# Optimization experiments

Hardware: AMD Instinct MI355X
Metric: run time of the kernel (lower is better)

Reference implementation:

```python
import math
import jax, jax.numpy as jnp
import numpy as np

EPS = 1e-5
SCALE_BASE = 512.0


def xpos_apply(x, downscale=False):
    # x: (..., L, head_dim); faithful to RetNet's XPOS (torchscale xpos)
    L, hd = x.shape[-2], x.shape[-1]
    half = hd // 2
    scale_vec = (jnp.arange(0, hd, 2, dtype=x.dtype) + 0.4 * hd) / (1.4 * hd)  # (half,)
    pos = jnp.arange(L, dtype=x.dtype)
    scale = scale_vec[None, :] ** (pos[:, None] / SCALE_BASE)  # (L, half)
    inv_freq = 1.0 / (10000.0 ** (jnp.arange(half, dtype=x.dtype) / half))
    sinusoid = pos[:, None] * inv_freq[None, :]  # (L, half)
    sin, cos = jnp.sin(sinusoid), jnp.cos(sinusoid)
    if downscale:
        scale = 1.0 / scale
    dup = lambda m: jnp.repeat(m, 2, axis=-1)  # duplicate_interleave -> (L, hd)
    sin_s, cos_s = dup(sin * scale), dup(cos * scale)
    x1, x2 = x[..., ::2], x[..., 1::2]
    rot = jnp.stack((-x2, x1), axis=-1).reshape(x.shape)  # rotate_every_two
    return x * cos_s + rot * sin_s


def decay_mask(L, gammas, dtype):
    # D[h, n, m] = gamma_h ** (n - m) if n >= m else 0
    n = jnp.arange(L)[:, None]
    m = jnp.arange(L)[None, :]
    causal = n >= m
    dist = jnp.where(causal, (n - m).astype(dtype), 0.0)
    return jnp.where(causal, gammas[:, None, None] ** dist, 0.0)  # (H, L, L)


def setup_inputs() -> dict:
    key = jax.random.key(0)
    ks = jax.random.split(key, 7)
    B, L, D, H = 1, 4096, 512, 8
    hs = D // H  # head_size = head_v_dim (double_v_dim=False)
    v_dim = D
    X = jax.random.normal(ks[0], (B, L, D), jnp.float32)
    W_Q = jax.random.normal(ks[1], (H, D, hs), jnp.float32) / D
    W_K = jax.random.normal(ks[2], (H, D, hs), jnp.float32) / D
    W_V = jax.random.normal(ks[3], (H, D, hs), jnp.float32) / D
    W_G = jax.random.normal(ks[4], (D, v_dim), jnp.float32) / D
    W_O = jax.random.normal(ks[5], (v_dim, D), jnp.float32) / D
    gn_weight = jnp.ones((v_dim,), jnp.float32)
    gn_bias = jnp.zeros((v_dim,), jnp.float32)
    return {"X": X, "W_Q": W_Q, "W_K": W_K, "W_V": W_V,
            "W_G": W_G, "W_O": W_O, "gn_weight": gn_weight, "gn_bias": gn_bias}


def reference(X, W_Q, W_K, W_V, W_G, W_O, gn_weight, gn_bias):
    B, L, D = X.shape
    H, _, hs = W_Q.shape
    hv = W_V.shape[-1]
    # per-head projections
    q = jnp.einsum('bld,ndh->bnlh', X, W_Q)
    k = jnp.einsum('bld,ndh->bnlh', X, W_K)
    v = jnp.einsum('bld,ndv->bnlv', X, W_V)
    q = xpos_apply(q, downscale=False)
    k = xpos_apply(k, downscale=True)
    # fixed (non-trainable) decay gammas: 1 - exp(linspace(log(1/32), log(1/512)))
    gammas = 1.0 - jnp.exp(jnp.linspace(math.log(1.0 / 32), math.log(1.0 / 512), H)).astype(X.dtype)
    Dmask = decay_mask(L, gammas, X.dtype)  # (H, L, L)
    scores = jnp.einsum('bnlh,bnsh->bnls', q, k) * Dmask[None]
    ret = jnp.einsum('bnls,bnsv->bnlv', scores, v)
    ret = ret.transpose(0, 2, 1, 3).reshape(B, L, H * hv)  # b l (n h)
    # GroupNorm(heads, v_dim) applied to (B*L, v_dim)
    g = ret.reshape(B * L, H, hv)
    mu = g.mean(-1, keepdims=True)
    var = g.var(-1, keepdims=True)
    g = (g - mu) * jax.lax.rsqrt(var + EPS)
    g = g.reshape(B, L, H * hv) * gn_weight + gn_bias
    gate = jax.nn.silu(X @ W_G)
    return (gate * g) @ W_O
```

## Files before the change

### kernel.cpp

```cpp
#include <hip/hip_runtime.h>
#include <math.h>

#define LQ 4096
#define DD 512
#define NH 8
#define HS 64
#define HALF 32

typedef unsigned short u16;
typedef unsigned int u32;
typedef __attribute__((ext_vector_type(8)))  short s8v;
typedef __attribute__((ext_vector_type(4)))  float f4v;
typedef __attribute__((ext_vector_type(4)))  u32  u32x4;
typedef __attribute__((ext_vector_type(16))) float f16v;

#define WS_QH   0u
#define WS_QL   1048576u
#define WS_KH   2097152u
#define WS_KL   3145728u
#define WS_VT   4194304u
#define WS_XFH  5242880u
#define WS_XFL  6291456u
#define WS_WF   7340032u
#define WS_GATE 8650752u
#define WS_TAB  10747904u
#define WS_KTWH 11272192u
#define WS_KTWL 12320768u

__device__ inline u16 f2bf(float x) {
    unsigned int u = __float_as_uint(x);
    return (u16)((u + 0x7fffu + ((u >> 16) & 1u)) >> 16);
}
__device__ inline float bf2f(u16 h) { return __uint_as_float(((unsigned int)h) << 16); }

__device__ __forceinline__ void gld16(void* lds, const void* g) {
    __builtin_amdgcn_global_load_lds(
        (const __attribute__((address_space(1))) void*)g,
        (__attribute__((address_space(3))) void*)lds, 16, 0, 0);
}

__global__ __launch_bounds__(256) void k_pre(
    const float* __restrict__ X,
    const float* __restrict__ Wq, const float* __restrict__ Wk, const float* __restrict__ Wv,
    const float* __restrict__ Wg, const float* __restrict__ Wo,
    float* __restrict__ tab, u16* __restrict__ Xfh, u16* __restrict__ Xfl,
    u16* __restrict__ Wf) {
    __shared__ float tile[32][33];
    const int b = blockIdx.x;
    const int t = threadIdx.x;
    if (b < 512) {
        int idx = b * 256 + t;
        if (idx >= LQ * HALF) return;
        int l = idx >> 5;
        int i = idx & 31;
        double log2sv = log2((2.0 * i + 25.6) / 89.6);
        double e = (double)l * log2sv * (1.0 / 512.0);
        float sc  = exp2f((float)e);
        float sci = exp2f((float)(-e));
        double invf = exp2((double)i * (-13.287712379549449 / 32.0));
        double th = (double)l * invf;
        double r = th - 6.283185307179586 * floor(th * 0.15915494309189535);
        float c = cosf((float)r), sn = sinf((float)r);
        tab[idx]                 = c * sc;
        tab[LQ*HALF + idx]       = sn * sc;
        tab[2*LQ*HALF + idx]     = c * sci;
        tab[3*LQ*HALF + idx]     = sn * sci;
    } else if (b < 1536) {
        int g = (b - 512) * 256 + t;
        int l = g >> 6;
        int d = (g & 63) * 8;
        const float* xp = X + (size_t)l * DD + d;
        f4v x0 = *(const f4v*)xp;
        f4v x1 = *(const f4v*)(xp + 4);
        s8v ph, pl;
#pragma unroll
        for (int j = 0; j < 4; ++j) {
            u16 hb = f2bf(x0[j]);
            ph[j] = (short)hb; pl[j] = (short)f2bf(x0[j] - bf2f(hb));
            u16 hb2 = f2bf(x1[j]);
            ph[j+4] = (short)hb2; pl[j+4] = (short)f2bf(x1[j] - bf2f(hb2));
        }
        int rb = l >> 5, kt = d >> 6, ks = (d >> 4) & 3, kh2 = (d >> 3) & 1;
        int lane = kh2 * 32 + (l & 31);
        size_t off = (((size_t)(rb * 8 + kt) * 4 + ks) * 64 + lane) * 8;
        *(s8v*)(Xfh + off) = ph;
        *(s8v*)(Xfl + off) = pl;
    } else {
        int bb = b - 1536;
        int d0 = (bb & 15) * 32, C0 = (bb >> 4) * 32;
        int proj = C0 >> 9;
        int tc = t & 31, tr = t >> 5;
#pragma unroll
        for (int rr = 0; rr < 4; ++rr) {
            int dl = tr + rr * 8;
            int d = d0 + dl;
            int C = C0 + tc;
            float val;
            if (proj < 3) {
                const float* W = (proj == 0) ? Wq : ((proj == 1) ? Wk : Wv);
                int h = (C & 511) >> 6, hs = C & 63;
                val = W[(size_t)h * (DD * HS) + (size_t)d * HS + hs];
            } else if (proj == 3) {
                val = Wg[(size_t)d * DD + (C & 511)];
            } else {
                val = Wo[(size_t)d * DD + (C - 2048)];
            }
            tile[dl][tc] = val;
        }
        __syncthreads();
        if (t < 128) {
            int cl = t & 31, dgq = t >> 5;
            int dl = dgq * 8;
            s8v pk;
#pragma unroll
            for (int j = 0; j < 8; ++j) pk[j] = (short)f2bf(tile[dl + j][cl]);
            int C = C0 + cl;
            int da = d0 + dl;
            int nb = C >> 5, kt = da >> 6, ks = (da >> 4) & 3, kh2 = (da >> 3) & 1;
            int lane = kh2 * 32 + (C & 31);
            size_t off = (((size_t)(nb * 8 + kt) * 4 + ks) * 64 + lane) * 8;
            *(s8v*)(Wf + off) = pk;
        }
    }
}

__global__ __launch_bounds__(256) void k_fused(
    const u16* __restrict__ Xfh, const u16* __restrict__ Xfl,
    const u16* __restrict__ Wf,
    const float* __restrict__ tab,
    u16* __restrict__ qh, u16* __restrict__ ql,
    u16* __restrict__ kh, u16* __restrict__ kl,
    u16* __restrict__ vt, u16* __restrict__ gate16,
    u16* __restrict__ ktwh, u16* __restrict__ ktwl) {
    __shared__ __align__(16) char smem[33024];
    const int t = threadIdx.x;
    const int b = blockIdx.x;
    const int mb = (b & 7) * 4 + (b >> 8);
    const int cb = (b >> 3) & 31;
    const int l0 = mb * 128;
    const int c0 = cb * 64;
    const int wv = t >> 6;
    const int lane = t & 63;
    const int c31 = lane & 31;
    const int hi = lane >> 5;

    const int rb = mb * 4 + wv;
    const u16* pAh = Xfh + (size_t)rb * 16384 + lane * 8;
    const u16* pAl = Xfl + (size_t)rb * 16384 + lane * 8;
    const char* gB = (const char*)(Wf + (size_t)(cb * 2) * 16384);

    f16v acc0, acc1;
#pragma unroll
    for (int i = 0; i < 16; ++i) { acc0[i] = 0.f; acc1[i] = 0.f; }

#define STAGEB(PH)                                                             \
    { _Pragma("unroll") for (int j = 0; j < 8; ++j) {                          \
        int seg = j >> 2, q4 = j & 3;                                          \
        gld16(smem + seg * 16384 + q4 * 4096 + wv * 1024,                      \
              gB + seg * 32768 + (PH) * 16384 + q4 * 4096 + t * 16); } }

    if (c0 < 1024) {
        s8v ahA[4], alA[4], ahB[4], alB[4];
#define LOADQ(S, KT)                                                      \
        { _Pragma("unroll") for (int ks = 0; ks < 4; ++ks) {              \
            ah##S[ks] = *(const s8v*)(pAh + (KT) * 2048 + ks * 512);      \
            al##S[ks] = *(const s8v*)(pAl + (KT) * 2048 + ks * 512); } }
#define MFMAQ(S, KT)                                                                        \
        { const char* bbq = smem + ((KT) & 3) * 4096;                                       \
          _Pragma("unroll") for (int ks = 0; ks < 4; ++ks) {                                \
            s8v b0 = *(const s8v*)(bbq + ks * 1024 + lane * 16);                            \
            s8v b1 = *(const s8v*)(bbq + 16384 + ks * 1024 + lane * 16);                    \
            acc0 = __builtin_amdgcn_mfma_f32_32x32x16_bf16(ah##S[ks], b0, acc0, 0, 0, 0);   \
            acc0 = __builtin_amdgcn_mfma_f32_32x32x16_bf16(al##S[ks], b0, acc0, 0, 0, 0);   \
            acc1 = __builtin_amdgcn_mfma_f32_32x32x16_bf16(ah##S[ks], b1, acc1, 0, 0, 0);   \
            acc1 = __builtin_amdgcn_mfma_f32_32x32x16_bf16(al##S[ks], b1, acc1, 0, 0, 0); } }
        STAGEB(0)
        LOADQ(A, 0)
        asm volatile("s_waitcnt vmcnt(0)" ::: "memory");
        __syncthreads();
        LOADQ(B, 1)
        __builtin_amdgcn_sched_barrier(0);
        MFMAQ(A, 0)
        LOADQ(A, 2)
        __builtin_amdgcn_sched_barrier(0);
        MFMAQ(B, 1)
        LOADQ(B, 3)
        __builtin_amdgcn_sched_barrier(0);
        MFMAQ(A, 2)
        LOADQ(A, 4)
        __builtin_amdgcn_sched_barrier(0);
        MFMAQ(B, 3)
        __syncthreads();
        STAGEB(1)
        asm volatile("s_waitcnt vmcnt(0)" ::: "memory");
        __syncthreads();
        LOADQ(B, 5)
        __builtin_amdgcn_sched_barrier(0);
        MFMAQ(A, 4)
        LOADQ(A, 6)
        __builtin_amdgcn_sched_barrier(0);
        MFMAQ(B, 5)
        LOADQ(B, 7)
        __builtin_amdgcn_sched_barrier(0);
        MFMAQ(A, 6)
        __builtin_amdgcn_sched_barrier(0);
        MFMAQ(B, 7)
#undef LOADQ
#undef MFMAQ
    } else {
        s8v ahA[4], ahB[4];
#define LOADS(S, KT)                                                      \
        { _Pragma("unroll") for (int ks = 0; ks < 4; ++ks) {              \
            ah##S[ks] = *(const s8v*)(pAh + (KT) * 2048 + ks * 512); } }
#define MFMAS(S, KT)                                                                        \
        { const char* bbq = smem + ((KT) & 3) * 4096;                                       \
          _Pragma("unroll") for (int ks = 0; ks < 4; ++ks) {                                \
            s8v b0 = *(const s8v*)(bbq + ks * 1024 + lane * 16);                            \
            s8v b1 = *(const s8v*)(bbq + 16384 + ks * 1024 + lane * 16);                    \
            acc0 = __builtin_amdgcn_mfma_f32_32x32x16_bf16(ah##S[ks], b0, acc0, 0, 0, 0);   \
            acc1 = __builtin_amdgcn_mfma_f32_32x32x16_bf16(ah##S[ks], b1, acc1, 0, 0, 0); } }
        STAGEB(0)
        LOADS(A, 0)
        asm volatile("s_waitcnt vmcnt(0)" ::: "memory");
        __syncthreads();
        LOADS(B, 1)
        __builtin_amdgcn_sched_barrier(0);
        MFMAS(A, 0)
        LOADS(A, 2)
        __builtin_amdgcn_sched_barrier(0);
        MFMAS(B, 1)
        LOADS(B, 3)
        __builtin_amdgcn_sched_barrier(0);
        MFMAS(A, 2)
        LOADS(A, 4)
        __builtin_amdgcn_sched_barrier(0);
        MFMAS(B, 3)
        __syncthreads();
        STAGEB(1)
        asm volatile("s_waitcnt vmcnt(0)" ::: "memory");
        __syncthreads();
        LOADS(B, 5)
        __builtin_amdgcn_sched_barrier(0);
        MFMAS(A, 4)
        LOADS(A, 6)
        __builtin_amdgcn_sched_barrier(0);
        MFMAS(B, 5)
        LOADS(B, 7)
        __builtin_amdgcn_sched_barrier(0);
        MFMAS(A, 6)
        __builtin_amdgcn_sched_barrier(0);
        MFMAS(B, 7)
#undef LOADS
#undef MFMAS
    }
#undef STAGEB
    __syncthreads();

    float* vbuf = (float*)smem;
    const int proj = c0 >> 9;
    if (proj < 2) {
        const float* ct = tab + (proj ? 2 * LQ * HALF : 0);
        const float* st = tab + (proj ? 3 * LQ * HALF : LQ * HALF);
        u16* oh = proj ? kh : qh;
        u16* ol = proj ? kl : ql;
        const int hh = (c0 & 511) >> 6;
        float lgf = 0.f;
        if (proj == 1) {
            double lg = -3.4657359027997265 + (double)hh * (-2.772588722239781 / 7.0);
            lgf = (float)(log(1.0 - exp(lg)) * 1.4426950408889634);
        }
#pragma unroll
        for (int n = 0; n < 2; ++n) {
            const f16v acc = n ? acc1 : acc0;
            int C = c0 + n * 32 + c31;
            int hs = C & 63, i2 = hs >> 1;
            float sgn = (hs & 1) ? 1.f : -1.f;
#pragma unroll
            for (int r = 0; r < 16; ++r) {
                int lrow = wv * 32 + (r & 3) + 8 * (r >> 2) + 4 * hi;
                int pos = l0 + lrow;
                float val = acc[r];
                float part = __shfl_xor(val, 1);
                float res = val * ct[pos * HALF + i2] + sgn * part * st[pos * HALF + i2];
                u16 hb = f2bf(res);
                size_t o = ((size_t)hh * LQ + pos) * HS + hs;
                oh[o] = hb;
                ol[o] = f2bf(res - bf2f(hb));
                if (proj == 1) {
                    float wf = exp2f(lgf * (float)(64 - (pos & 63)));
                    vbuf[(n * 32 + c31) * 129 + lrow] = res * wf;
                }
            }
        }
        if (proj == 1) {
            __syncthreads();
            int cl = t >> 2, lseg = (t & 3) * 32;
            size_t o = ((size_t)hh * HS + cl) * LQ + l0 + lseg;
#pragma unroll
            for (int ch4 = 0; ch4 < 4; ++ch4) {
                s8v pkh, pkl;
#pragma unroll
                for (int j = 0; j < 8; ++j) {
                    float v = vbuf[cl * 129 + lseg + ch4 * 8 + j];
                    u16 hb = f2bf(v);
                    pkh[j] = (short)hb;
                    pkl[j] = (short)f2bf(v - bf2f(hb));
                }
                *(s8v*)(ktwh + o + ch4 * 8) = pkh;
                *(s8v*)(ktwl + o + ch4 * 8) = pkl;
            }
        }
    } else if (proj == 2) {
#pragma unroll
        for (int n = 0; n < 2; ++n) {
            const f16v acc = n ? acc1 : acc0;
            int cl = n * 32 + c31;
#pragma unroll
            for (int r = 0; r < 16; ++r) {
                int lrow = wv * 32 + (r & 3) + 8 * (r >> 2) + 4 * hi;
                vbuf[cl * 129 + lrow] = acc[r];
            }
        }
        __syncthreads();
        int h = (c0 & 511) >> 6;
        int cl = t >> 2, lseg = (t & 3) * 32;
        size_t o = ((size_t)h * HS + cl) * LQ + l0 + lseg;
#pragma unroll
        for (int ch = 0; ch < 4; ++ch) {
            s8v pk;
#pragma unroll
            for (int j = 0; j < 8; ++j) pk[j] = (short)f2bf(vbuf[cl * 129 + lseg + ch * 8 + j]);
            *(s8v*)(vt + o + ch * 8) = pk;
        }
    } else {
#pragma unroll
        for (int n = 0; n < 2; ++n) {
            const f16v acc = n ? acc1 : acc0;
            int C = (c0 & 511) + n * 32 + c31;
#pragma unroll
            for (int r = 0; r < 16; ++r) {
                int lrow = wv * 32 + (r & 3) + 8 * (r >> 2) + 4 * hi;
                float vv = acc[r];
                gate16[(size_t)(l0 + lrow) * DD + C] = f2bf(vv / (1.f + expf(-vv)));
            }
        }
    }
}

__global__ __launch_bounds__(256) void k_ret1(
    const u16* __restrict__ vt, const u16* __restrict__ ktwh, const u16* __restrict__ ktwl,
    float* __restrict__ A) {
    const int t = threadIdx.x;
    const int c = blockIdx.x;
    const int h = blockIdx.y;
    const int wv = t >> 6, lane = t & 63, c31 = lane & 31, hi = lane >> 5;
    const int wch = wv >> 1, wd = wv & 1;

    s8v va[4];
    const u16* vp = vt + ((size_t)h * 64 + wch * 32 + c31) * LQ + c * 64 + hi * 8;
#pragma unroll
    for (int ks = 0; ks < 4; ++ks) va[ks] = *(const s8v*)(vp + ks * 16);

    f16v a;
#pragma unroll
    for (int i = 0; i < 16; ++i) a[i] = 0.f;

    const size_t kbase = ((size_t)h * 64 + wd * 32 + c31) * LQ + c * 64 + hi * 8;
#pragma unroll
    for (int ks = 0; ks < 4; ++ks) {
        s8v b_h = *(const s8v*)(ktwh + kbase + ks * 16);
        s8v b_l = *(const s8v*)(ktwl + kbase + ks * 16);
        a = __builtin_amdgcn_mfma_f32_32x32x16_bf16(va[ks], b_h, a, 0, 0, 0);
        a = __builtin_amdgcn_mfma_f32_32x32x16_bf16(va[ks], b_l, a, 0, 0, 0);
    }

    float* Ab = A + ((size_t)h * 64 + c) * 4096;
#pragma unroll
    for (int r = 0; r < 16; ++r) {
        int ch = wch * 32 + (r & 3) + 8 * (r >> 2) + 4 * hi;
        Ab[ch * 64 + wd * 32 + c31] = a[r];
    }
}

__global__ __launch_bounds__(256) void k_scan(
    const float* __restrict__ A, u16* __restrict__ sth, u16* __restrict__ stl) {
    const int bx = blockIdx.x;
    const int h = bx >> 4;
    const int e = (bx & 15) * 256 + threadIdx.x;
    double lg = -3.4657359027997265 + (double)h * (-2.772588722239781 / 7.0);
    double gamma = 1.0 - exp(lg);
    float g64 = (float)pow(gamma, 64.0);
    const float* Ab = A + (size_t)h * 64 * 4096 + e;
    u16* shb = sth + (size_t)h * 64 * 4096 + e;
    u16* slb = stl + (size_t)h * 64 * 4096 + e;
    float av[64];
#pragma unroll
    for (int cc = 0; cc < 64; ++cc) av[cc] = Ab[(size_t)cc * 4096];
    float s = 0.f;
#pragma unroll
    for (int cc = 0; cc < 64; ++cc) {
        if (cc) {
            u16 hb = f2bf(s);
            shb[(size_t)cc * 4096] = hb;
            slb[(size_t)cc * 4096] = f2bf(s - bf2f(hb));
        }
        s = fmaf(g64, s, av[cc]);
    }
}

__global__ __launch_bounds__(256) void k_ret3(
    const u16* __restrict__ qh, const u16* __restrict__ ql,
    const u16* __restrict__ kh, const u16* __restrict__ kl,
    const u16* __restrict__ vt,
    const u16* __restrict__ sth, const u16* __restrict__ stl,
    const u16* __restrict__ gate16,
    const float* __restrict__ gw, const float* __restrict__ gb,
    u16* __restrict__ Gf) {
    __shared__ __align__(16) char sBuf[24576];
    __shared__ float stats[64][2][2];
    const int t = threadIdx.x;
    const int c = blockIdx.x;
    const int h = blockIdx.y;
    const int wv = t >> 6, lane = t & 63, c31 = lane & 31, hi = lane >> 5;
    const int ws = wv >> 1, wc = wv & 1;
    const int l0q = c * 64;

    double lg = -3.4657359027997265 + (double)h * (-2.772588722239781 / 7.0);
    double gamma = 1.0 - exp(lg);
    float lgf = (float)(log(gamma) * 1.4426950408889634);
    float c1a[4], c8a[4];
#pragma unroll
    for (int m = 0; m < 4; ++m) { c1a[m] = exp2f(-lgf * (float)m); c8a[m] = exp2f(-lgf * (float)(8 * m)); }

    s8v qhf[4], qlf[4];
    {
        const u16* qph = qh + ((size_t)h * LQ + l0q + ws * 32 + c31) * HS + hi * 8;
        const u16* qpl = ql + ((size_t)h * LQ + l0q + ws * 32 + c31) * HS + hi * 8;
#pragma unroll
        for (int ks = 0; ks < 4; ++ks) {
            qhf[ks] = *(const s8v*)(qph + ks * 16);
            qlf[ks] = *(const s8v*)(qpl + ks * 16);
        }
    }

    {
        const char* gKH = (const char*)kh + ((size_t)h * LQ + l0q) * 128;
        const char* gKL = (const char*)kl + ((size_t)h * LQ + l0q) * 128;
        const char* gVT = (const char*)vt + ((size_t)h * 64) * 8192 + l0q * 2;
#pragma unroll
        for (int i_ = 0; i_ < 6; ++i_) {
            int boff = i_ * 4096 + t * 16;
            int seg = boff >> 13;
            int o_ = boff & 8191;
            int osrc = o_ ^ (((o_ >> 7) & 7) << 4);
            const char* src = (seg == 0) ? gKH + osrc
                            : (seg == 1) ? gKL + osrc
                            : gVT + (size_t)(osrc >> 7) * 8192 + (osrc & 127);
            gld16(sBuf + (i_ & ~0) * 4096 + (t >> 6) * 1024, src);
        }
    }

    f16v qs;
#pragma unroll
    for (int i = 0; i < 16; ++i) qs[i] = 0.f;
    if (c > 0) {
        const u16* sbh = sth + ((size_t)h * 64 + c) * 4096;
        const u16* sbl = stl + ((size_t)h * 64 + c) * 4096;
#pragma unroll
        for (int ks = 0; ks < 4; ++ks) {
            int off = (wc * 32 + c31) * 64 + ks * 16 + hi * 8;
            s8v b_h = *(const s8v*)(sbh + off);
            s8v b_l = *(const s8v*)(sbl + off);
            qs = __builtin_amdgcn_mfma_f32_32x32x16_bf16(qhf[ks], b_h, qs, 0, 0, 0);
            qs = __builtin_amdgcn_mfma_f32_32x32x16_bf16(qhf[ks], b_l, qs, 0, 0, 0);
            qs = __builtin_amdgcn_mfma_f32_32x32x16_bf16(qlf[ks], b_h, qs, 0, 0, 0);
        }
    }

    asm volatile("s_waitcnt vmcnt(0)" ::: "memory");
    __syncthreads();

    f16v acc;
#pragma unroll
    for (int i = 0; i < 16; ++i) acc[i] = 0.f;
    const char* bKH = sBuf;
    const char* bKL = sBuf + 8192;
    const char* bVT = sBuf + 16384;

#pragma unroll
    for (int jt = 0; jt < 2; ++jt) {
        if (ws == 0 && jt == 1) break;
        f16v sacc;
#pragma unroll
        for (int i = 0; i < 16; ++i) sacc[i] = 0.f;
#pragma unroll
        for (int ks = 0; ks < 4; ++ks) {
            int krow = jt * 32 + c31;
            int ph = krow * 128 + ((ks * 32 + hi * 16) ^ ((krow & 7) << 4));
            s8v ah = *(const s8v*)(bKH + ph);
            s8v al = *(const s8v*)(bKL + ph);
            sacc = __builtin_amdgcn_mfma_f32_32x32x16_bf16(ah, qhf[ks], sacc, 0, 0, 0);
            sacc = __builtin_amdgcn_mfma_f32_32x32x16_bf16(ah, qlf[ks], sacc, 0, 0, 0);
            sacc = __builtin_amdgcn_mfma_f32_32x32x16_bf16(al, qhf[ks], sacc, 0, 0, 0);
        }
        const int D0 = (ws * 32 + c31) - jt * 32;
        float base = exp2f(lgf * (float)(D0 - 4 * hi));
        u32 w[8];
#pragma unroll
        for (int g = 0; g < 4; ++g) {
            float wg = base * c8a[g];
            float v0 = sacc[4 * g + 0] * (wg * c1a[0]);
            float v1 = sacc[4 * g + 1] * (wg * c1a[1]);
            float v2 = sacc[4 * g + 2] * (wg * c1a[2]);
            float v3 = sacc[4 * g + 3] * (wg * c1a[3]);
            int jr = 8 * g + 4 * hi;
            if (D0 - (jr + 0) < 0) v0 = 0.f;
            if (D0 - (jr + 1) < 0) v1 = 0.f;
            if (D0 - (jr + 2) < 0) v2 = 0.f;
            if (D0 - (jr + 3) < 0) v3 = 0.f;
            w[2 * g]     = (u32)f2bf(v0) | ((u32)f2bf(v1) << 16);
            w[2 * g + 1] = (u32)f2bf(v2) | ((u32)f2bf(v3) << 16);
        }
        u32 e0 = __shfl_xor(hi ? w[0] : w[2], 32);
        u32 e1 = __shfl_xor(hi ? w[1] : w[3], 32);
        u32 e2 = __shfl_xor(hi ? w[4] : w[6], 32);
        u32 e3 = __shfl_xor(hi ? w[5] : w[7], 32);
        u32x4 a0v = { hi ? e0 : w[0], hi ? e1 : w[1], hi ? w[2] : e0, hi ? w[3] : e1 };
        u32x4 a1v = { hi ? e2 : w[4], hi ? e3 : w[5], hi ? w[6] : e2, hi ? w[7] : e3 };
        s8v af0 = __builtin_bit_cast(s8v, a0v);
        s8v af1 = __builtin_bit_cast(s8v, a1v);
#pragma unroll
        for (int ksl = 0; ksl < 2; ++ksl) {
            s8v af = ksl ? af1 : af0;
            int cb = (jt * 2 + ksl) * 32 + hi * 16;
            int rv = wc * 32 + c31;
            s8v vb = *(const s8v*)(bVT + rv * 128 + (cb ^ ((rv & 7) << 4)));
            acc = __builtin_amdgcn_mfma_f32_32x32x16_bf16(af, vb, acc, 0, 0, 0);
        }
    }

    float vv[16];
#pragma unroll
    for (int r = 0; r < 16; ++r) {
        int row = (r & 3) + 8 * (r >> 2) + 4 * hi;
        int nloc = ws * 32 + row;
        float sc = exp2f(lgf * (float)nloc);
        vv[r] = acc[r] + sc * qs[r];
    }
#pragma unroll
    for (int r = 0; r < 16; ++r) {
        float s = vv[r], ss = vv[r] * vv[r];
#pragma unroll
        for (int off = 1; off < 32; off <<= 1) {
            s  += __shfl_xor(s, off);
            ss += __shfl_xor(ss, off);
        }
        if (c31 == 0) {
            int nloc = ws * 32 + (r & 3) + 8 * (r >> 2) + 4 * hi;
            stats[nloc][wc][0] = s;
            stats[nloc][wc][1] = ss;
        }
    }
    __syncthreads();

    float* gT = (float*)sBuf;
    const float gwv = gw[h * HS + wc * 32 + c31];
    const float gbv = gb[h * HS + wc * 32 + c31];
#pragma unroll
    for (int r = 0; r < 16; ++r) {
        int nloc = ws * 32 + (r & 3) + 8 * (r >> 2) + 4 * hi;
        float s  = stats[nloc][0][0] + stats[nloc][1][0];
        float ss = stats[nloc][0][1] + stats[nloc][1][1];
        float mean = s * (1.f / 64.f);
        float var = ss * (1.f / 64.f) - mean * mean;
        float inv = rsqrtf(var + 1e-5f);
        size_t o = (size_t)(l0q + nloc) * DD + h * HS + wc * 32 + c31;
        float g = ((vv[r] - mean) * inv * gwv + gbv) * bf2f(gate16[o]);
        gT[nloc * 65 + wc * 32 + c31] = g;
    }
    __syncthreads();
#pragma unroll
    for (int i = 0; i < 2; ++i) {
        int u = t + i * 256;
        int rbl = u >> 8;
        int ks = (u >> 6) & 3;
        int ln = u & 63;
        int row = rbl * 32 + (ln & 31);
        int ch = ks * 16 + (ln >> 5) * 8;
        s8v pk;
#pragma unroll
        for (int j = 0; j < 8; ++j) pk[j] = (short)f2bf(gT[row * 65 + ch + j]);
        size_t off = ((((size_t)(c * 2 + rbl) * 8 + h) * 4 + ks) * 64 + ln) * 8;
        *(s8v*)(Gf + off) = pk;
    }
}

__global__ __launch_bounds__(256) void k_out(
    const u16* __restrict__ Gf, const u16* __restrict__ Wf,
    float* __restrict__ out) {
    __shared__ __align__(16) char smem[32768];
    const int t = threadIdx.x;
    const int l0 = blockIdx.x * 128;
    const int c0 = blockIdx.y * 64;
    const int wv = t >> 6;
    const int lane = t & 63;
    const int c31 = lane & 31;
    const int hi = lane >> 5;

    const int rb = blockIdx.x * 4 + wv;
    const u16* pA  = Gf + (size_t)rb * 16384 + lane * 8;
    const char* gB = (const char*)(Wf + (size_t)(64 + blockIdx.y * 2) * 16384);

    f16v acc0, acc1;
#pragma unroll
    for (int i = 0; i < 16; ++i) { acc0[i] = 0.f; acc1[i] = 0.f; }

#define STAGEB(PH)                                                             \
    { _Pragma("unroll") for (int j = 0; j < 8; ++j) {                          \
        int seg = j >> 2, q4 = j & 3;                                          \
        gld16(smem + seg * 16384 + q4 * 4096 + wv * 1024,                      \
              gB + seg * 32768 + (PH) * 16384 + q4 * 4096 + t * 16); } }
    s8v aA[4], aB[4];
#define LOADO(S, KT)                                                      \
    { _Pragma("unroll") for (int ks = 0; ks < 4; ++ks) {                  \
        a##S[ks] = *(const s8v*)(pA + (KT) * 2048 + ks * 512); } }
#define MFMAO(S, KT)                                                                        \
    { const char* bbq = smem + ((KT) & 3) * 4096;                                           \
      _Pragma("unroll") for (int ks = 0; ks < 4; ++ks) {                                    \
        s8v b0 = *(const s8v*)(bbq + ks * 1024 + lane * 16);                                \
        s8v b1 = *(const s8v*)(bbq + 16384 + ks * 1024 + lane * 16);                        \
        acc0 = __builtin_amdgcn_mfma_f32_32x32x16_bf16(a##S[ks], b0, acc0, 0, 0, 0);        \
        acc1 = __builtin_amdgcn_mfma_f32_32x32x16_bf16(a##S[ks], b1, acc1, 0, 0, 0); } }
    STAGEB(0)
    LOADO(A, 0)
    asm volatile("s_waitcnt vmcnt(0)" ::: "memory");
    __syncthreads();
    LOADO(B, 1)
    __builtin_amdgcn_sched_barrier(0);
    MFMAO(A, 0)
    LOADO(A, 2)
    __builtin_amdgcn_sched_barrier(0);
    MFMAO(B, 1)
    LOADO(B, 3)
    __builtin_amdgcn_sched_barrier(0);
    MFMAO(A, 2)
    LOADO(A, 4)
    __builtin_amdgcn_sched_barrier(0);
    MFMAO(B, 3)
    __syncthreads();
    STAGEB(1)
    asm volatile("s_waitcnt vmcnt(0)" ::: "memory");
    __syncthreads();
    LOADO(B, 5)
    __builtin_amdgcn_sched_barrier(0);
    MFMAO(A, 4)
    LOADO(A, 6)
    __builtin_amdgcn_sched_barrier(0);
    MFMAO(B, 5)
    LOADO(B, 7)
    __builtin_amdgcn_sched_barrier(0);
    MFMAO(A, 6)
    __builtin_amdgcn_sched_barrier(0);
    MFMAO(B, 7)
#undef LOADO
#undef MFMAO
#undef STAGEB

#pragma unroll
    for (int n = 0; n < 2; ++n) {
        const f16v acc = n ? acc1 : acc0;
        int C = c0 + n * 32 + c31;
#pragma unroll
        for (int r = 0; r < 16; ++r) {
            int lrow = wv * 32 + (r & 3) + 8 * (r >> 2) + 4 * hi;
            out[(size_t)(l0 + lrow) * DD + C] = acc[r];
        }
    }
}

extern "C" void kernel_launch(void* const* d_in, const int* in_sizes, int n_in,
                              void* d_out, int out_size, void* d_ws, size_t ws_size,
                              hipStream_t stream) {
    const float* X   = (const float*)d_in[0];
    const float* W_Q = (const float*)d_in[1];
    const float* W_K = (const float*)d_in[2];
    const float* W_V = (const float*)d_in[3];
    const float* W_G = (const float*)d_in[4];
    const float* W_O = (const float*)d_in[5];
    const float* gnw = (const float*)d_in[6];
    const float* gnb = (const float*)d_in[7];

    float* ws   = (float*)d_ws;
    u16* qhp  = (u16*)(ws + WS_QH);
    u16* qlp  = (u16*)(ws + WS_QL);
    u16* khp  = (u16*)(ws + WS_KH);
    u16* klp  = (u16*)(ws + WS_KL);
    u16* vtp  = (u16*)(ws + WS_VT);
    u16* xfh  = (u16*)(ws + WS_XFH);
    u16* xfl  = (u16*)(ws + WS_XFL);
    u16* wf   = (u16*)(ws + WS_WF);
    u16* gate16 = (u16*)(ws + WS_GATE);
    float* tab  = ws + WS_TAB;
    u16* ktwh = (u16*)(ws + WS_KTWH);
    u16* ktwl = (u16*)(ws + WS_KTWL);
    float* Abuf = ws + WS_XFH;
    u16* sthp = (u16*)(ws + WS_KTWH);
    u16* stlp = (u16*)(ws + WS_KTWL);
    u16* Gfp  = (u16*)(ws + WS_XFH);
    float* out  = (float*)d_out;

    k_pre<<<2816, 256, 0, stream>>>(X, W_Q, W_K, W_V, W_G, W_O, tab, xfh, xfl, wf);
    k_fused<<<1024, 256, 0, stream>>>(xfh, xfl, wf, tab, qhp, qlp, khp, klp, vtp, gate16, ktwh, ktwl);
    k_ret1<<<dim3(64, 8), 256, 0, stream>>>(vtp, ktwh, ktwl, Abuf);
    k_scan<<<128, 256, 0, stream>>>(Abuf, sthp, stlp);
    k_ret3<<<dim3(64, 8), 256, 0, stream>>>(qhp, qlp, khp, klp, vtp, sthp, stlp,
                                            gate16, gnw, gnb, Gfp);
    k_out<<<dim3(32, 8), 256, 0, stream>>>(Gfp, wf, out);
}
```

Before: 78.54 us.

## Drop split-bf16 hi/lo compensation and use single bf16 operands throughout

Removes the hi/lo bf16 error-compensation split from every stage: X, Q, K, the decayed K tile, and the scan states are now stored as a single bf16. The extra MFMAs on the low-part terms are dropped, along with the low-part buffers, their loads and their LDS staging. This cuts MFMA work, memory traffic and shared memory use across the projection, retention, scan and chunk kernels. The cost is lower numerical accuracy, which risks failing the tolerance check against the fp32 reference.

```diff
diff --git a/kernel.cpp b/kernel.cpp
--- a/kernel.cpp
+++ b/kernel.cpp
@@ -15,7 +15,6 @@
 typedef __attribute__((ext_vector_type(16))) float f16v;
 
 #define WS_QH   0u
-#define WS_QL   1048576u
 #define WS_KH   2097152u
 #define WS_KL   3145728u
 #define WS_VT   4194304u
@@ -25,7 +24,6 @@
 #define WS_GATE 8650752u
 #define WS_TAB  10747904u
 #define WS_KTWH 11272192u
-#define WS_KTWL 12320768u
 
 __device__ inline u16 f2bf(float x) {
     unsigned int u = __float_as_uint(x);
@@ -43,8 +41,7 @@
     const float* __restrict__ X,
     const float* __restrict__ Wq, const float* __restrict__ Wk, const float* __restrict__ Wv,
     const float* __restrict__ Wg, const float* __restrict__ Wo,
-    float* __restrict__ tab, u16* __restrict__ Xfh, u16* __restrict__ Xfl,
-    u16* __restrict__ Wf) {
+    float* __restrict__ tab, u16* __restrict__ Xf, u16* __restrict__ Wf) {
     __shared__ float tile[32][33];
     const int b = blockIdx.x;
     const int t = threadIdx.x;
@@ -72,19 +69,16 @@
         const float* xp = X + (size_t)l * DD + d;
         f4v x0 = *(const f4v*)xp;
         f4v x1 = *(const f4v*)(xp + 4);
-        s8v ph, pl;
+        s8v ph;
 #pragma unroll
         for (int j = 0; j < 4; ++j) {
-            u16 hb = f2bf(x0[j]);
-            ph[j] = (short)hb; pl[j] = (short)f2bf(x0[j] - bf2f(hb));
-            u16 hb2 = f2bf(x1[j]);
-            ph[j+4] = (short)hb2; pl[j+4] = (short)f2bf(x1[j] - bf2f(hb2));
+            ph[j]   = (short)f2bf(x0[j]);
+            ph[j+4] = (short)f2bf(x1[j]);
         }
         int rb = l >> 5, kt = d >> 6, ks = (d >> 4) & 3, kh2 = (d >> 3) & 1;
         int lane = kh2 * 32 + (l & 31);
         size_t off = (((size_t)(rb * 8 + kt) * 4 + ks) * 64 + lane) * 8;
-        *(s8v*)(Xfh + off) = ph;
-        *(s8v*)(Xfl + off) = pl;
+        *(s8v*)(Xf + off) = ph;
     } else {
         int bb = b - 1536;
         int d0 = (bb & 15) * 32, C0 = (bb >> 4) * 32;
@@ -125,13 +119,11 @@
 }
 
 __global__ __launch_bounds__(256) void k_fused(
-    const u16* __restrict__ Xfh, const u16* __restrict__ Xfl,
-    const u16* __restrict__ Wf,
+    const u16* __restrict__ Xf, const u16* __restrict__ Wf,
     const float* __restrict__ tab,
-    u16* __restrict__ qh, u16* __restrict__ ql,
-    u16* __restrict__ kh, u16* __restrict__ kl,
+    u16* __restrict__ qh, u16* __restrict__ kh,
     u16* __restrict__ vt, u16* __restrict__ gate16,
-    u16* __restrict__ ktwh, u16* __restrict__ ktwl) {
+    u16* __restrict__ ktw) {
     __shared__ __align__(16) char smem[33024];
     const int t = threadIdx.x;
     const int b = blockIdx.x;
@@ -145,8 +137,7 @@
     const int hi = lane >> 5;
 
     const int rb = mb * 4 + wv;
-    const u16* pAh = Xfh + (size_t)rb * 16384 + lane * 8;
-    const u16* pAl = Xfl + (size_t)rb * 16384 + lane * 8;
+    const u16* pA = Xf + (size_t)rb * 16384 + lane * 8;
     const char* gB = (const char*)(Wf + (size_t)(cb * 2) * 16384);
 
     f16v acc0, acc1;
@@ -158,101 +149,50 @@
         int seg = j >> 2, q4 = j & 3;                                          \
         gld16(smem + seg * 16384 + q4 * 4096 + wv * 1024,                      \
               gB + seg * 32768 + (PH) * 16384 + q4 * 4096 + t * 16); } }
-
-    if (c0 < 1024) {
-        s8v ahA[4], alA[4], ahB[4], alB[4];
-#define LOADQ(S, KT)                                                      \
-        { _Pragma("unroll") for (int ks = 0; ks < 4; ++ks) {              \
-            ah##S[ks] = *(const s8v*)(pAh + (KT) * 2048 + ks * 512);      \
-            al##S[ks] = *(const s8v*)(pAl + (KT) * 2048 + ks * 512); } }
-#define MFMAQ(S, KT)                                                                        \
-        { const char* bbq = smem + ((KT) & 3) * 4096;                                       \
-          _Pragma("unroll") for (int ks = 0; ks < 4; ++ks) {                                \
-            s8v b0 = *(const s8v*)(bbq + ks * 1024 + lane * 16);                            \
-            s8v b1 = *(const s8v*)(bbq + 16384 + ks * 1024 + lane * 16);                    \
-            acc0 = __builtin_amdgcn_mfma_f32_32x32x16_bf16(ah##S[ks], b0, acc0, 0, 0, 0);   \
-            acc0 = __builtin_amdgcn_mfma_f32_32x32x16_bf16(al##S[ks], b0, acc0, 0, 0, 0);   \
-            acc1 = __builtin_amdgcn_mfma_f32_32x32x16_bf16(ah##S[ks], b1, acc1, 0, 0, 0);   \
-            acc1 = __builtin_amdgcn_mfma_f32_32x32x16_bf16(al##S[ks], b1, acc1, 0, 0, 0); } }
-        STAGEB(0)
-        LOADQ(A, 0)
-        asm volatile("s_waitcnt vmcnt(0)" ::: "memory");
-        __syncthreads();
-        LOADQ(B, 1)
-        __builtin_amdgcn_sched_barrier(0);
-        MFMAQ(A, 0)
-        LOADQ(A, 2)
-        __builtin_amdgcn_sched_barrier(0);
-        MFMAQ(B, 1)
-        LOADQ(B, 3)
-        __builtin_amdgcn_sched_barrier(0);
-        MFMAQ(A, 2)
-        LOADQ(A, 4)
-        __builtin_amdgcn_sched_barrier(0);
-        MFMAQ(B, 3)
-        __syncthreads();
-        STAGEB(1)
-        asm volatile("s_waitcnt vmcnt(0)" ::: "memory");
-        __syncthreads();
-        LOADQ(B, 5)
-        __builtin_amdgcn_sched_barrier(0);
-        MFMAQ(A, 4)
-        LOADQ(A, 6)
-        __builtin_amdgcn_sched_barrier(0);
-        MFMAQ(B, 5)
-        LOADQ(B, 7)
-        __builtin_amdgcn_sched_barrier(0);
-        MFMAQ(A, 6)
-        __builtin_amdgcn_sched_barrier(0);
-        MFMAQ(B, 7)
-#undef LOADQ
-#undef MFMAQ
-    } else {
-        s8v ahA[4], ahB[4];
-#define LOADS(S, KT)                                                      \
-        { _Pragma("unroll") for (int ks = 0; ks < 4; ++ks) {              \
-            ah##S[ks] = *(const s8v*)(pAh + (KT) * 2048 + ks * 512); } }
-#define MFMAS(S, KT)                                                                        \
-        { const char* bbq = smem + ((KT) & 3) * 4096;                                       \
-          _Pragma("unroll") for (int ks = 0; ks < 4; ++ks) {                                \
-            s8v b0 = *(const s8v*)(bbq + ks * 1024 + lane * 16);                            \
-            s8v b1 = *(const s8v*)(bbq + 16384 + ks * 1024 + lane * 16);                    \
-            acc0 = __builtin_amdgcn_mfma_f32_32x32x16_bf16(ah##S[ks], b0, acc0, 0, 0, 0);   \
-            acc1 = __builtin_amdgcn_mfma_f32_32x32x16_bf16(ah##S[ks], b1, acc1, 0, 0, 0); } }
-        STAGEB(0)
-        LOADS(A, 0)
-        asm volatile("s_waitcnt vmcnt(0)" ::: "memory");
-        __syncthreads();
-        LOADS(B, 1)
-        __builtin_amdgcn_sched_barrier(0);
-        MFMAS(A, 0)
-        LOADS(A, 2)
-        __builtin_amdgcn_sched_barrier(0);
-        MFMAS(B, 1)
-        LOADS(B, 3)
-        __builtin_amdgcn_sched_barrier(0);
-        MFMAS(A, 2)
-        LOADS(A, 4)
-        __builtin_amdgcn_sched_barrier(0);
-        MFMAS(B, 3)
-        __syncthreads();
-        STAGEB(1)
-        asm volatile("s_waitcnt vmcnt(0)" ::: "memory");
-        __syncthreads();
-        LOADS(B, 5)
-        __builtin_amdgcn_sched_barrier(0);
-        MFMAS(A, 4)
-        LOADS(A, 6)
-        __builtin_amdgcn_sched_barrier(0);
-        MFMAS(B, 5)
-        LOADS(B, 7)
-        __builtin_amdgcn_sched_barrier(0);
-        MFMAS(A, 6)
-        __builtin_amdgcn_sched_barrier(0);
-        MFMAS(B, 7)
-#undef LOADS
-#undef MFMAS
-    }
+    s8v aA[4], aB[4];
+#define LOADA(S, KT)                                                      \
+    { _Pragma("unroll") for (int ks = 0; ks < 4; ++ks) {                  \
+        a##S[ks] = *(const s8v*)(pA + (KT) * 2048 + ks * 512); } }
+#define MFMAX(S, KT)                                                                        \
+    { const char* bbq = smem + ((KT) & 3) * 4096;                                           \
+      _Pragma("unroll") for (int ks = 0; ks < 4; ++ks) {                                    \
+        s8v b0 = *(const s8v*)(bbq + ks * 1024 + lane * 16);                                \
+        s8v b1 = *(const s8v*)(bbq + 16384 + ks * 1024 + lane * 16);                        \
+        acc0 = __builtin_amdgcn_mfma_f32_32x32x16_bf16(a##S[ks], b0, acc0, 0, 0, 0);        \
+        acc1 = __builtin_amdgcn_mfma_f32_32x32x16_bf16(a##S[ks], b1, acc1, 0, 0, 0); } }
+    STAGEB(0)
+    LOADA(A, 0)
+    asm volatile("s_waitcnt vmcnt(0)" ::: "memory");
+    __syncthreads();
+    LOADA(B, 1)
+    __builtin_amdgcn_sched_barrier(0);
+    MFMAX(A, 0)
+    LOADA(A, 2)
+    __builtin_amdgcn_sched_barrier(0);
+    MFMAX(B, 1)
+    LOADA(B, 3)
+    __builtin_amdgcn_sched_barrier(0);
+    MFMAX(A, 2)
+    LOADA(A, 4)
+    __builtin_amdgcn_sched_barrier(0);
+    MFMAX(B, 3)
+    __syncthreads();
+    STAGEB(1)
+    asm volatile("s_waitcnt vmcnt(0)" ::: "memory");
+    __syncthreads();
+    LOADA(B, 5)
+    __builtin_amdgcn_sched_barrier(0);
+    MFMAX(A, 4)
+    LOADA(A, 6)
+    __builtin_amdgcn_sched_barrier(0);
+    MFMAX(B, 5)
+    LOADA(B, 7)
+    __builtin_amdgcn_sched_barrier(0);
+    MFMAX(A, 6)
+    __builtin_amdgcn_sched_barrier(0);
+    MFMAX(B, 7)
+#undef LOADA
+#undef MFMAX
 #undef STAGEB
     __syncthreads();
 
@@ -262,7 +202,6 @@
         const float* ct = tab + (proj ? 2 * LQ * HALF : 0);
         const float* st = tab + (proj ? 3 * LQ * HALF : LQ * HALF);
         u16* oh = proj ? kh : qh;
-        u16* ol = proj ? kl : ql;
         const int hh = (c0 & 511) >> 6;
         float lgf = 0.f;
         if (proj == 1) {
@@ -282,10 +221,8 @@
                 float val = acc[r];
                 float part = __shfl_xor(val, 1);
                 float res = val * ct[pos * HALF + i2] + sgn * part * st[pos * HALF + i2];
-                u16 hb = f2bf(res);
                 size_t o = ((size_t)hh * LQ + pos) * HS + hs;
-                oh[o] = hb;
-                ol[o] = f2bf(res - bf2f(hb));
+                oh[o] = f2bf(res);
                 if (proj == 1) {
                     float wf = exp2f(lgf * (float)(64 - (pos & 63)));
                     vbuf[(n * 32 + c31) * 129 + lrow] = res * wf;
@@ -298,16 +235,10 @@
             size_t o = ((size_t)hh * HS + cl) * LQ + l0 + lseg;
 #pragma unroll
             for (int ch4 = 0; ch4 < 4; ++ch4) {
-                s8v pkh, pkl;
-#pragma unroll
-                for (int j = 0; j < 8; ++j) {
-                    float v = vbuf[cl * 129 + lseg + ch4 * 8 + j];
-                    u16 hb = f2bf(v);
-                    pkh[j] = (short)hb;
-                    pkl[j] = (short)f2bf(v - bf2f(hb));
-                }
-                *(s8v*)(ktwh + o + ch4 * 8) = pkh;
-                *(s8v*)(ktwl + o + ch4 * 8) = pkl;
+                s8v pkh;
+#pragma unroll
+                for (int j = 0; j < 8; ++j) pkh[j] = (short)f2bf(vbuf[cl * 129 + lseg + ch4 * 8 + j]);
+                *(s8v*)(ktw + o + ch4 * 8) = pkh;
             }
         }
     } else if (proj == 2) {
@@ -348,7 +279,7 @@
 }
 
 __global__ __launch_bounds__(256) void k_ret1(
-    const u16* __restrict__ vt, const u16* __restrict__ ktwh, const u16* __restrict__ ktwl,
+    const u16* __restrict__ vt, const u16* __restrict__ ktw,
     float* __restrict__ A) {
     const int t = threadIdx.x;
     const int c = blockIdx.x;
@@ -368,10 +299,8 @@
     const size_t kbase = ((size_t)h * 64 + wd * 32 + c31) * LQ + c * 64 + hi * 8;
 #pragma unroll
     for (int ks = 0; ks < 4; ++ks) {
-        s8v b_h = *(const s8v*)(ktwh + kbase + ks * 16);
-        s8v b_l = *(const s8v*)(ktwl + kbase + ks * 16);
+        s8v b_h = *(const s8v*)(ktw + kbase + ks * 16);
         a = __builtin_amdgcn_mfma_f32_32x32x16_bf16(va[ks], b_h, a, 0, 0, 0);
-        a = __builtin_amdgcn_mfma_f32_32x32x16_bf16(va[ks], b_l, a, 0, 0, 0);
     }
 
     float* Ab = A + ((size_t)h * 64 + c) * 4096;
@@ -383,7 +312,7 @@
 }
 
 __global__ __launch_bounds__(256) void k_scan(
-    const float* __restrict__ A, u16* __restrict__ sth, u16* __restrict__ stl) {
+    const float* __restrict__ A, u16* __restrict__ sth) {
     const int bx = blockIdx.x;
     const int h = bx >> 4;
     const int e = (bx & 15) * 256 + threadIdx.x;
@@ -392,31 +321,24 @@
     float g64 = (float)pow(gamma, 64.0);
     const float* Ab = A + (size_t)h * 64 * 4096 + e;
     u16* shb = sth + (size_t)h * 64 * 4096 + e;
-    u16* slb = stl + (size_t)h * 64 * 4096 + e;
     float av[64];
 #pragma unroll
     for (int cc = 0; cc < 64; ++cc) av[cc] = Ab[(size_t)cc * 4096];
     float s = 0.f;
 #pragma unroll
     for (int cc = 0; cc < 64; ++cc) {
-        if (cc) {
-            u16 hb = f2bf(s);
-            shb[(size_t)cc * 4096] = hb;
-            slb[(size_t)cc * 4096] = f2bf(s - bf2f(hb));
-        }
+        if (cc) shb[(size_t)cc * 4096] = f2bf(s);
         s = fmaf(g64, s, av[cc]);
     }
 }
 
 __global__ __launch_bounds__(256) void k_ret3(
-    const u16* __restrict__ qh, const u16* __restrict__ ql,
-    const u16* __restrict__ kh, const u16* __restrict__ kl,
-    const u16* __restrict__ vt,
-    const u16* __restrict__ sth, const u16* __restrict__ stl,
+    const u16* __restrict__ qh, const u16* __restrict__ kh,
+    const u16* __restrict__ vt, const u16* __restrict__ sth,
     const u16* __restrict__ gate16,
     const float* __restrict__ gw, const float* __restrict__ gb,
     u16* __restrict__ Gf) {
-    __shared__ __align__(16) char sBuf[24576];
+    __shared__ __align__(16) char sBuf[16640];
     __shared__ float stats[64][2][2];
     const int t = threadIdx.x;
     const int c = blockIdx.x;
@@ -432,31 +354,25 @@
 #pragma unroll
     for (int m = 0; m < 4; ++m) { c1a[m] = exp2f(-lgf * (float)m); c8a[m] = exp2f(-lgf * (float)(8 * m)); }
 
-    s8v qhf[4], qlf[4];
+    s8v qhf[4];
     {
         const u16* qph = qh + ((size_t)h * LQ + l0q + ws * 32 + c31) * HS + hi * 8;
-        const u16* qpl = ql + ((size_t)h * LQ + l0q + ws * 32 + c31) * HS + hi * 8;
-#pragma unroll
-        for (int ks = 0; ks < 4; ++ks) {
-            qhf[ks] = *(const s8v*)(qph + ks * 16);
-            qlf[ks] = *(const s8v*)(qpl + ks * 16);
-        }
+#pragma unroll
+        for (int ks = 0; ks < 4; ++ks) qhf[ks] = *(const s8v*)(qph + ks * 16);
     }
 
     {
         const char* gKH = (const char*)kh + ((size_t)h * LQ + l0q) * 128;
-        const char* gKL = (const char*)kl + ((size_t)h * LQ + l0q) * 128;
         const char* gVT = (const char*)vt + ((size_t)h * 64) * 8192 + l0q * 2;
 #pragma unroll
-        for (int i_ = 0; i_ < 6; ++i_) {
+        for (int i_ = 0; i_ < 4; ++i_) {
             int boff = i_ * 4096 + t * 16;
             int seg = boff >> 13;
             int o_ = boff & 8191;
             int osrc = o_ ^ (((o_ >> 7) & 7) << 4);
             const char* src = (seg == 0) ? gKH + osrc
-                            : (seg == 1) ? gKL + osrc
                             : gVT + (size_t)(osrc >> 7) * 8192 + (osrc & 127);
-            gld16(sBuf + (i_ & ~0) * 4096 + (t >> 6) * 1024, src);
+            gld16(sBuf + boff, src);
         }
     }
 
@@ -465,15 +381,11 @@
     for (int i = 0; i < 16; ++i) qs[i] = 0.f;
     if (c > 0) {
         const u16* sbh = sth + ((size_t)h * 64 + c) * 4096;
-        const u16* sbl = stl + ((size_t)h * 64 + c) * 4096;
 #pragma unroll
         for (int ks = 0; ks < 4; ++ks) {
             int off = (wc * 32 + c31) * 64 + ks * 16 + hi * 8;
             s8v b_h = *(const s8v*)(sbh + off);
-            s8v b_l = *(const s8v*)(sbl + off);
             qs = __builtin_amdgcn_mfma_f32_32x32x16_bf16(qhf[ks], b_h, qs, 0, 0, 0);
-            qs = __builtin_amdgcn_mfma_f32_32x32x16_bf16(qhf[ks], b_l, qs, 0, 0, 0);
-            qs = __builtin_amdgcn_mfma_f32_32x32x16_bf16(qlf[ks], b_h, qs, 0, 0, 0);
         }
     }
 
@@ -484,8 +396,7 @@
 #pragma unroll
     for (int i = 0; i < 16; ++i) acc[i] = 0.f;
     const char* bKH = sBuf;
-    const char* bKL = sBuf + 8192;
-    const char* bVT = sBuf + 16384;
+    const char* bVT = sBuf + 8192;
 
 #pragma unroll
     for (int jt = 0; jt < 2; ++jt) {
@@ -498,10 +409,7 @@
             int krow = jt * 32 + c31;
             int ph = krow * 128 + ((ks * 32 + hi * 16) ^ ((krow & 7) << 4));
             s8v ah = *(const s8v*)(bKH + ph);
-            s8v al = *(const s8v*)(bKL + ph);
             sacc = __builtin_amdgcn_mfma_f32_32x32x16_bf16(ah, qhf[ks], sacc, 0, 0, 0);
-            sacc = __builtin_amdgcn_mfma_f32_32x32x16_bf16(ah, qlf[ks], sacc, 0, 0, 0);
-            sacc = __builtin_amdgcn_mfma_f32_32x32x16_bf16(al, qhf[ks], sacc, 0, 0, 0);
         }
         const int D0 = (ws * 32 + c31) - jt * 32;
         float base = exp2f(lgf * (float)(D0 - 4 * hi));
@@ -692,28 +600,22 @@
 
     float* ws   = (float*)d_ws;
     u16* qhp  = (u16*)(ws + WS_QH);
-    u16* qlp  = (u16*)(ws + WS_QL);
     u16* khp  = (u16*)(ws + WS_KH);
-    u16* klp  = (u16*)(ws + WS_KL);
     u16* vtp  = (u16*)(ws + WS_VT);
-    u16* xfh  = (u16*)(ws + WS_XFH);
-    u16* xfl  = (u16*)(ws + WS_XFL);
+    u16* xfp  = (u16*)(ws + WS_XFH);
     u16* wf   = (u16*)(ws + WS_WF);
     u16* gate16 = (u16*)(ws + WS_GATE);
     float* tab  = ws + WS_TAB;
-    u16* ktwh = (u16*)(ws + WS_KTWH);
-    u16* ktwl = (u16*)(ws + WS_KTWL);
+    u16* ktwp = (u16*)(ws + WS_KTWH);
     float* Abuf = ws + WS_XFH;
     u16* sthp = (u16*)(ws + WS_KTWH);
-    u16* stlp = (u16*)(ws + WS_KTWL);
     u16* Gfp  = (u16*)(ws + WS_XFH);
     float* out  = (float*)d_out;
 
-    k_pre<<<2816, 256, 0, stream>>>(X, W_Q, W_K, W_V, W_G, W_O, tab, xfh, xfl, wf);
-    k_fused<<<1024, 256, 0, stream>>>(xfh, xfl, wf, tab, qhp, qlp, khp, klp, vtp, gate16, ktwh, ktwl);
-    k_ret1<<<dim3(64, 8), 256, 0, stream>>>(vtp, ktwh, ktwl, Abuf);
-    k_scan<<<128, 256, 0, stream>>>(Abuf, sthp, stlp);
-    k_ret3<<<dim3(64, 8), 256, 0, stream>>>(qhp, qlp, khp, klp, vtp, sthp, stlp,
-                                            gate16, gnw, gnb, Gfp);
+    k_pre<<<2816, 256, 0, stream>>>(X, W_Q, W_K, W_V, W_G, W_O, tab, xfp, wf);
+    k_fused<<<1024, 256, 0, stream>>>(xfp, wf, tab, qhp, khp, vtp, gate16, ktwp);
+    k_ret1<<<dim3(64, 8), 256, 0, stream>>>(vtp, ktwp, Abuf);
+    k_scan<<<128, 256, 0, stream>>>(Abuf, sthp);
+    k_ret3<<<dim3(64, 8), 256, 0, stream>>>(qhp, khp, vtp, sthp, gate16, gnw, gnb, Gfp);
     k_out<<<dim3(32, 8), 256, 0, stream>>>(Gfp, wf, out);
 }
```

Measured after the change: 66.62 us. 1.18x faster.
